# Performance work log

Measured on AMD Instinct MI355X. Metric: run time of the kernel, lower is better.

Reference implementation:

```python
import jax, jax.numpy as jnp
import numpy as np

D_MODEL = 1024
N_HEAD = 16
D_HEAD = D_MODEL // N_HEAD
NEG = -1e9


def setup_inputs() -> dict:
    key = jax.random.key(0)
    ks = jax.random.split(key, 11)
    B, T, C = 4, 2048, D_MODEL
    s = 1.0 / np.sqrt(C)
    return {
        "q": jax.random.normal(ks[0], (B, T, C), jnp.float32),
        "k": jax.random.normal(ks[1], (B, T, C), jnp.float32),
        "v": jax.random.normal(ks[2], (B, T, C), jnp.float32),
        "w_q": jax.random.normal(ks[3], (C, C), jnp.float32) * s,
        "b_q": jnp.zeros((C,), jnp.float32),
        "w_k": jax.random.normal(ks[4], (C, C), jnp.float32) * s,
        "b_k": jnp.zeros((C,), jnp.float32),
        "w_v": jax.random.normal(ks[5], (C, C), jnp.float32) * s,
        "b_v": jnp.zeros((C,), jnp.float32),
        "w_o": jax.random.normal(ks[6], (C, C), jnp.float32) * s,
        "b_o": jnp.zeros((C,), jnp.float32),
    }


def reference(q, k, v, w_q, b_q, w_k, b_k, w_v, b_v, w_o, b_o):
    B, T, C = q.shape
    # projections; weights stored as [in, out]
    qh = (q @ w_q + b_q).reshape(B, T, N_HEAD, D_HEAD).transpose(0, 2, 1, 3)
    kh = (k @ w_k + b_k).reshape(B, T, N_HEAD, D_HEAD).transpose(0, 2, 1, 3)
    vh = (v @ w_v + b_v).reshape(B, T, N_HEAD, D_HEAD).transpose(0, 2, 1, 3)
    scores = jnp.einsum("bhqd,bhkd->bhqk", qh, kh) / jnp.sqrt(
        jnp.asarray(D_HEAD, qh.dtype))
    causal = jnp.tril(jnp.ones((T, T), dtype=bool))  # [T,T]
    scores = jnp.where(causal[None, None], scores, NEG)
    attn = jax.nn.softmax(scores, axis=-1)
    out = jnp.einsum("bhqk,bhkd->bhqd", attn, vh)
    out = out.transpose(0, 2, 1, 3).reshape(B, T, C)
    return out @ w_o + b_o
```

## Files before the change

kernel.cpp:

```cpp
#include <hip/hip_runtime.h>
#include <hip/hip_bf16.h>
#include <cstdint>
#include <cstddef>

#define DEVI static __device__ __forceinline__

typedef __attribute__((ext_vector_type(8))) short short8;
typedef __attribute__((ext_vector_type(4))) float f32x4;

typedef __attribute__((address_space(1))) const unsigned int as1c_uint;
typedef __attribute__((address_space(3))) unsigned int as3_uint;

constexpr int Bn = 4, Tn = 2048, Cn = 1024, Hn = 16, Dn = 64;
constexpr int Mtot = Bn * Tn;
#define QSCALE (0.125f * 1.44269504088896340736f)

DEVI unsigned short f2bf(float f) {
  unsigned u = __float_as_uint(f);
  u += 0x7fffu + ((u >> 16) & 1u);
  return (unsigned short)(u >> 16);
}
DEVI unsigned short f2bf_t(float f) {
  return (unsigned short)(__float_as_uint(f) >> 16);
}

DEVI void async16(const void* g, void* l) {
  __builtin_amdgcn_global_load_lds((as1c_uint*)g, (as3_uint*)l, 16, 0, 0);
}

__global__ __launch_bounds__(256) void cvt3_kernel(
    const float4* __restrict__ i0, const float4* __restrict__ i1,
    const float4* __restrict__ i2, ushort4* __restrict__ o0,
    ushort4* __restrict__ o1, ushort4* __restrict__ o2, int n4, int zoff) {
  const int z = blockIdx.y + zoff;
  const float4* in = z == 0 ? i0 : z == 1 ? i1 : i2;
  ushort4* out = z == 0 ? o0 : z == 1 ? o1 : o2;
  const int stride = gridDim.x * blockDim.x;
  for (int i = blockIdx.x * blockDim.x + threadIdx.x; i < n4; i += stride) {
    float4 v = in[i];
    ushort4 o;
    o.x = f2bf(v.x); o.y = f2bf(v.y); o.z = f2bf(v.z); o.w = f2bf(v.w);
    out[i] = o;
  }
}

__global__ __launch_bounds__(256) void transpose_cvt4(
    const float* __restrict__ w0, const float* __restrict__ w1,
    const float* __restrict__ w2, const float* __restrict__ w3,
    unsigned short* __restrict__ o0, unsigned short* __restrict__ o1,
    unsigned short* __restrict__ o2, unsigned short* __restrict__ o3) {
  __shared__ float tile[32][33];
  const int z = blockIdx.z;
  const float* w = z == 0 ? w0 : z == 1 ? w1 : z == 2 ? w2 : w3;
  unsigned short* wT = z == 0 ? o0 : z == 1 ? o1 : z == 2 ? o2 : o3;
  int n0 = blockIdx.x * 32, k0 = blockIdx.y * 32;
  int tx = threadIdx.x, ty = threadIdx.y;
#pragma unroll
  for (int r = 0; r < 32; r += 8)
    tile[ty + r][tx] = w[(size_t)(k0 + ty + r) * Cn + n0 + tx];
  __syncthreads();
#pragma unroll
  for (int r = 0; r < 32; r += 8)
    wT[(size_t)(n0 + ty + r) * Cn + k0 + tx] = f2bf(tile[tx][ty + r]);
}

DEVI void gemm_core(const unsigned short* A, const unsigned short* BT, int K,
                    int m0, int n0, int tid, f32x4 acc[4][4]) {
  __shared__ unsigned short Alds[128 * 32];
  __shared__ unsigned short Blds[128 * 32];
  const int lane = tid & 63, w = tid >> 6;
  const int wm = w >> 1, wn = w & 1;
  const int l15 = lane & 15, l4 = lane >> 4;

  for (int k0 = 0; k0 < K; k0 += 32) {
    __syncthreads();
#pragma unroll
    for (int t = 0; t < 2; ++t) {
      int chunk = w * 2 + t;
      int row = chunk * 16 + (lane >> 2);
      int seg = lane & 3;
      async16(A + (size_t)(m0 + row) * K + k0 + seg * 8, &Alds[chunk * 512]);
      async16(BT + (size_t)(n0 + row) * K + k0 + seg * 8, &Blds[chunk * 512]);
    }
    __syncthreads();

    short8 af[4], bf[4];
#pragma unroll
    for (int i = 0; i < 4; ++i) {
      af[i] = *(const short8*)&Alds[(wm * 64 + i * 16 + l15) * 32 + l4 * 8];
      bf[i] = *(const short8*)&Blds[(wn * 64 + i * 16 + l15) * 32 + l4 * 8];
    }
#pragma unroll
    for (int i = 0; i < 4; ++i)
#pragma unroll
      for (int j = 0; j < 4; ++j)
        acc[i][j] = __builtin_amdgcn_mfma_f32_16x16x32_bf16(af[i], bf[j], acc[i][j], 0, 0, 0);
  }
}

__global__ __launch_bounds__(256) void gemm_qkv(
    const unsigned short* __restrict__ Aq, const unsigned short* __restrict__ Ak,
    const unsigned short* __restrict__ Av, const unsigned short* __restrict__ Bq,
    const unsigned short* __restrict__ Bk, const unsigned short* __restrict__ Bv,
    const float* __restrict__ bq, const float* __restrict__ bk,
    const float* __restrict__ bv, unsigned short* __restrict__ oq,
    unsigned short* __restrict__ ok, unsigned short* __restrict__ ov, int zoff) {
  const int z = blockIdx.z + zoff;
  const unsigned short* A = z == 0 ? Aq : z == 1 ? Ak : Av;
  const unsigned short* BT = z == 0 ? Bq : z == 1 ? Bk : Bv;
  const float* bias = z == 0 ? bq : z == 1 ? bk : bv;
  unsigned short* o = z == 0 ? oq : z == 1 ? ok : ov;

  const int tid = threadIdx.x;
  const int lane = tid & 63, w = tid >> 6;
  const int wm = w >> 1, wn = w & 1;
  const int l15 = lane & 15, l4 = lane >> 4;
  const int m0 = blockIdx.x * 128, n0 = blockIdx.y * 128;

  const f32x4 zf = {0.f, 0.f, 0.f, 0.f};
  f32x4 acc[4][4];
#pragma unroll
  for (int i = 0; i < 4; ++i)
#pragma unroll
    for (int j = 0; j < 4; ++j) acc[i][j] = zf;

  gemm_core(A, BT, Cn, m0, n0, tid, acc);

#pragma unroll
  for (int j = 0; j < 4; ++j) {
    int n = n0 + wn * 64 + j * 16 + l15;
    float bvl = bias[n];
    int h = n >> 6, d = n & 63;
#pragma unroll
    for (int i = 0; i < 4; ++i) {
      int mbase = m0 + wm * 64 + i * 16 + l4 * 4;
      if (z < 2) {
        float scale = z == 0 ? QSCALE : 1.f;
#pragma unroll
        for (int r = 0; r < 4; ++r) {
          int m = mbase + r;
          int b = m >> 11, t = m & 2047;
          o[((size_t)((b * Hn + h) * Tn + t)) * Dn + d] = f2bf((acc[i][j][r] + bvl) * scale);
        }
      } else {
        int b = mbase >> 11, t0 = mbase & 2047;
        ushort4 pk;
        pk.x = f2bf(acc[i][j][0] + bvl);
        pk.y = f2bf(acc[i][j][1] + bvl);
        pk.z = f2bf(acc[i][j][2] + bvl);
        pk.w = f2bf(acc[i][j][3] + bvl);
        *(ushort4*)&o[((size_t)((b * Hn + h) * Dn + d)) * Tn + t0] = pk;
      }
    }
  }
}

__global__ __launch_bounds__(256) void gemm_out(const unsigned short* __restrict__ A,
                                                const unsigned short* __restrict__ BT,
                                                const float* __restrict__ bias,
                                                float* __restrict__ o) {
  const int tid = threadIdx.x;
  const int lane = tid & 63, w = tid >> 6;
  const int wm = w >> 1, wn = w & 1;
  const int l15 = lane & 15, l4 = lane >> 4;
  const int m0 = blockIdx.x * 128, n0 = blockIdx.y * 128;

  const f32x4 zf = {0.f, 0.f, 0.f, 0.f};
  f32x4 acc[4][4];
#pragma unroll
  for (int i = 0; i < 4; ++i)
#pragma unroll
    for (int j = 0; j < 4; ++j) acc[i][j] = zf;

  gemm_core(A, BT, Cn, m0, n0, tid, acc);

#pragma unroll
  for (int j = 0; j < 4; ++j) {
    int n = n0 + wn * 64 + j * 16 + l15;
    float bvl = bias[n];
#pragma unroll
    for (int i = 0; i < 4; ++i) {
      int mbase = m0 + wm * 64 + i * 16 + l4 * 4;
#pragma unroll
      for (int r = 0; r < 4; ++r)
        o[(size_t)(mbase + r) * Cn + n] = acc[i][j][r] + bvl;
    }
  }
}

__global__ __launch_bounds__(512) void attn_kernel(const unsigned short* __restrict__ qh,
                                                   const unsigned short* __restrict__ kh,
                                                   const unsigned short* __restrict__ vt,
                                                   unsigned short* __restrict__ obf) {
  __shared__ unsigned short Ks[2][64 * 64];
  __shared__ unsigned short Vs[2][64 * 64];
  __shared__ unsigned short Ps[8][16 * 72];

  const int tid = threadIdx.x, lane = tid & 63, w = tid >> 6;
  const int l15 = lane & 15, l4 = lane >> 4;
  const int swz = l15 & 7;

  const int bid = blockIdx.x;
  const int j = bid >> 3;
  const int bh = (bid & 7) * 8 + (j & 7);
  const int pair = j >> 3;
  const unsigned short* qb = qh + (size_t)bh * Tn * Dn;
  const unsigned short* kb = kh + (size_t)bh * Tn * Dn;
  const unsigned short* vb = vt + (size_t)bh * Dn * Tn;
  const int b = bh >> 4, h = bh & 15;

  const int srow = lane >> 3, sslot = (lane & 7) ^ (lane >> 3);

  const f32x4 z = {0.f, 0.f, 0.f, 0.f};
  const short ob = (short)0x3F80;
  const short8 ones = {ob, ob, ob, ob, ob, ob, ob, ob};

#pragma unroll 1
  for (int half = 0; half < 2; ++half) {
    const int qt = half == 0 ? pair : 15 - pair;
    const int q0 = qt * 128;
    const int qrow = q0 + w * 16 + l15;

    short8 qf0 = *(const short8*)(qb + (size_t)qrow * Dn + l4 * 8);
    short8 qf1 = *(const short8*)(qb + (size_t)qrow * Dn + 32 + l4 * 8);

    f32x4 o[4];
#pragma unroll
    for (int nd = 0; nd < 4; ++nd) o[nd] = z;
    f32x4 osum = z;

    const int nt = (q0 >> 6) + 2;
    const int ntw = ((q0 + w * 16 + 15) >> 6) + 1;

    {
      const unsigned short* ksrc = kb + (size_t)(w * 8 + srow) * Dn + sslot * 8;
      const unsigned short* vsrc = vb + (size_t)(w * 8 + srow) * Tn + sslot * 8;
      async16(ksrc, &Ks[0][w * 512]);
      async16(vsrc, &Vs[0][w * 512]);
    }

#pragma unroll 1
    for (int t = 0; t < nt; ++t) {
      const int cur = t & 1;
      if (t + 1 < nt) {
        const int kv1 = (t + 1) * 64;
        const unsigned short* ksrc = kb + (size_t)(kv1 + w * 8 + srow) * Dn + sslot * 8;
        const unsigned short* vsrc = vb + (size_t)(w * 8 + srow) * Tn + kv1 + sslot * 8;
        async16(ksrc, &Ks[cur ^ 1][w * 512]);
        async16(vsrc, &Vs[cur ^ 1][w * 512]);
        asm volatile("s_waitcnt vmcnt(2)" ::: "memory");
      } else {
        asm volatile("s_waitcnt vmcnt(0)" ::: "memory");
      }
      __builtin_amdgcn_s_barrier();
      __builtin_amdgcn_sched_barrier(0);

      if (t < ntw) {
        const unsigned short* Kc = &Ks[cur][0];
        const unsigned short* Vc = &Vs[cur][0];

        f32x4 s[4];
#pragma unroll
        for (int ni = 0; ni < 4; ++ni) s[ni] = z;
        __builtin_amdgcn_s_setprio(1);
#pragma unroll
        for (int ni = 0; ni < 4; ++ni) {
          const int rb = (ni * 16 + l15) * 64;
          short8 kf0 = *(const short8*)&Kc[rb + ((l4 ^ swz) * 8)];
          short8 kf1 = *(const short8*)&Kc[rb + (((4 + l4) ^ swz) * 8)];
          s[ni] = __builtin_amdgcn_mfma_f32_16x16x32_bf16(kf0, qf0, s[ni], 0, 0, 0);
          s[ni] = __builtin_amdgcn_mfma_f32_16x16x32_bf16(kf1, qf1, s[ni], 0, 0, 0);
        }
        __builtin_amdgcn_s_setprio(0);

        short8 vf[8];
#pragma unroll
        for (int nd = 0; nd < 4; ++nd) {
          const int rb = (nd * 16 + l15) * 64;
          vf[nd * 2]     = *(const short8*)&Vc[rb + ((l4 ^ swz) * 8)];
          vf[nd * 2 + 1] = *(const short8*)&Vc[rb + (((4 + l4) ^ swz) * 8)];
        }

        const int kq = qrow - t * 64;
        const bool edge = (t * 64 + 63 > q0 + w * 16);
        if (!edge) {
#pragma unroll
          for (int ni = 0; ni < 4; ++ni) {
            ushort4 pk;
#pragma unroll
            for (int r = 0; r < 4; ++r)
              ((unsigned short*)&pk)[r] = f2bf_t(__builtin_amdgcn_exp2f(s[ni][r]));
            *(ushort4*)&Ps[w][l15 * 72 + ni * 16 + l4 * 4] = pk;
          }
        } else {
#pragma unroll
          for (int ni = 0; ni < 4; ++ni) {
            ushort4 pk;
#pragma unroll
            for (int r = 0; r < 4; ++r) {
              float e = __builtin_amdgcn_exp2f(s[ni][r]);
              if ((ni * 16 + l4 * 4 + r) > kq) e = 0.f;
              ((unsigned short*)&pk)[r] = f2bf_t(e);
            }
            *(ushort4*)&Ps[w][l15 * 72 + ni * 16 + l4 * 4] = pk;
          }
        }
        asm volatile("s_waitcnt lgkmcnt(0)" ::: "memory");
        __builtin_amdgcn_sched_barrier(0);

        short8 pf0 = *(const short8*)&Ps[w][l15 * 72 + l4 * 8];
        short8 pf1 = *(const short8*)&Ps[w][l15 * 72 + 32 + l4 * 8];
        __builtin_amdgcn_s_setprio(1);
        osum = __builtin_amdgcn_mfma_f32_16x16x32_bf16(pf0, ones, osum, 0, 0, 0);
        osum = __builtin_amdgcn_mfma_f32_16x16x32_bf16(pf1, ones, osum, 0, 0, 0);
#pragma unroll
        for (int nd = 0; nd < 4; ++nd) {
          o[nd] = __builtin_amdgcn_mfma_f32_16x16x32_bf16(pf0, vf[nd * 2], o[nd], 0, 0, 0);
          o[nd] = __builtin_amdgcn_mfma_f32_16x16x32_bf16(pf1, vf[nd * 2 + 1], o[nd], 0, 0, 0);
        }
        __builtin_amdgcn_s_setprio(0);
      }

      __builtin_amdgcn_sched_barrier(0);
      __builtin_amdgcn_s_barrier();
    }

#pragma unroll
    for (int r = 0; r < 4; ++r) {
      float inv = __builtin_amdgcn_rcpf(osum[r]);
      int tq = q0 + w * 16 + l4 * 4 + r;
      size_t base = ((size_t)(b * Tn + tq)) * Cn + h * 64;
#pragma unroll
      for (int nd = 0; nd < 4; ++nd)
        obf[base + nd * 16 + l15] = f2bf(o[nd][r] * inv);
    }
  }
}

extern "C" void kernel_launch(void* const* d_in, const int* in_sizes, int n_in,
                              void* d_out, int out_size, void* d_ws, size_t ws_size,
                              hipStream_t stream) {
  const float* q   = (const float*)d_in[0];
  const float* k   = (const float*)d_in[1];
  const float* v   = (const float*)d_in[2];
  const float* w_q = (const float*)d_in[3];
  const float* b_q = (const float*)d_in[4];
  const float* w_k = (const float*)d_in[5];
  const float* b_k = (const float*)d_in[6];
  const float* w_v = (const float*)d_in[7];
  const float* b_v = (const float*)d_in[8];
  const float* w_o = (const float*)d_in[9];
  const float* b_o = (const float*)d_in[10];

  char* ws = (char*)d_ws;
  const size_t MB = 1u << 20;
  const bool big = ws_size >= 104 * MB;
  const int n4 = Mtot * Cn / 4;
  dim3 gg(Mtot / 128, Cn / 128, 1);

  unsigned short *xq, *xk, *xv, *qhp, *khp, *vtp, *wqT, *wkT, *wvT, *woT;
  if (big) {
    xq  = (unsigned short*)(ws);
    xk  = (unsigned short*)(ws + 16 * MB);
    xv  = (unsigned short*)(ws + 32 * MB);
    qhp = (unsigned short*)(ws + 48 * MB);
    khp = (unsigned short*)(ws + 64 * MB);
    vtp = (unsigned short*)(ws + 80 * MB);
    wqT = (unsigned short*)(ws + 96 * MB);
    wkT = (unsigned short*)(ws + 98 * MB);
    wvT = (unsigned short*)(ws + 100 * MB);
    woT = (unsigned short*)(ws + 102 * MB);
  } else {
    xq = xk = xv = (unsigned short*)(ws);
    wqT = (unsigned short*)(ws + 16 * MB);
    wkT = (unsigned short*)(ws + 18 * MB);
    wvT = (unsigned short*)(ws + 20 * MB);
    woT = (unsigned short*)(ws + 22 * MB);
    qhp = (unsigned short*)(ws + 24 * MB);
    khp = (unsigned short*)(ws + 40 * MB);
    vtp = (unsigned short*)(ws + 56 * MB);
  }
  unsigned short* aout = xq;

  transpose_cvt4<<<dim3(32, 32, 4), dim3(32, 8), 0, stream>>>(
      w_q, w_k, w_v, w_o, wqT, wkT, wvT, woT);

  if (big) {
    cvt3_kernel<<<dim3(2048, 3), 256, 0, stream>>>(
        (const float4*)q, (const float4*)k, (const float4*)v,
        (ushort4*)xq, (ushort4*)xk, (ushort4*)xv, n4, 0);
    dim3 g3(Mtot / 128, Cn / 128, 3);
    gemm_qkv<<<g3, 256, 0, stream>>>(xq, xk, xv, wqT, wkT, wvT,
                                     b_q, b_k, b_v, qhp, khp, vtp, 0);
  } else {
    for (int z = 0; z < 3; ++z) {
      cvt3_kernel<<<dim3(2048, 1), 256, 0, stream>>>(
          (const float4*)q, (const float4*)k, (const float4*)v,
          (ushort4*)xq, (ushort4*)xq, (ushort4*)xq, n4, z);
      gemm_qkv<<<gg, 256, 0, stream>>>(xq, xq, xq, wqT, wkT, wvT,
                                       b_q, b_k, b_v, qhp, khp, vtp, z);
    }
  }

  attn_kernel<<<512, 512, 0, stream>>>(qhp, khp, vtp, aout);

  gemm_out<<<gg, 256, 0, stream>>>(aout, woT, b_o, (float*)d_out);
}
```

Before: 182.4 us.

## Replace GEMM core with 256x256 double-buffered swizzled-LDS tile kernel

Replaces the 128x128 single-buffered GEMM core with a 256x256 tile per 512-thread block. It uses a 64-wide K step, double-buffered async LDS staging with XOR-swizzled columns, prefetch two stages ahead, and s_setprio around the MFMA bursts. Block IDs are remapped so neighbouring blocks share tiles. The aim is more data reuse per byte loaded, fewer bank conflicts, and load latency hidden behind compute. The cost is heavy register and LDS use (128 KB per block) and fewer blocks: 128 per GEMM, or 384 for the fused QKV launch.

```diff
diff --git a/kernel.cpp b/kernel.cpp
--- a/kernel.cpp
+++ b/kernel.cpp
@@ -64,41 +64,92 @@
     wT[(size_t)(n0 + ty + r) * Cn + k0 + tx] = f2bf(tile[tx][ty + r]);
 }
 
-DEVI void gemm_core(const unsigned short* A, const unsigned short* BT, int K,
-                    int m0, int n0, int tid, f32x4 acc[4][4]) {
-  __shared__ unsigned short Alds[128 * 32];
-  __shared__ unsigned short Blds[128 * 32];
+DEVI void stage256(const unsigned short* __restrict__ g, int ld, int m0, int k0,
+                   unsigned short* lds, int w, int lane) {
+#pragma unroll
+  for (int j = 0; j < 4; ++j) {
+    int s = j * 512 + w * 64 + lane;
+    int row = s >> 3;
+    int col = ((s & 7) ^ (row & 7)) * 8;
+    async16(g + (size_t)(m0 + row) * ld + k0 + col,
+            lds + (size_t)(j * 512 + w * 64) * 8);
+  }
+}
+
+DEVI void gemm8p_core(const unsigned short* __restrict__ A,
+                      const unsigned short* __restrict__ BT, int K,
+                      int m0, int n0, int tid, f32x4 (&acc)[8][4]) {
+  __shared__ unsigned short As[2][256 * 64];
+  __shared__ unsigned short Bs[2][256 * 64];
   const int lane = tid & 63, w = tid >> 6;
-  const int wm = w >> 1, wn = w & 1;
+  const int wm = w >> 2, wn = w & 3;
   const int l15 = lane & 15, l4 = lane >> 4;
-
-  for (int k0 = 0; k0 < K; k0 += 32) {
-    __syncthreads();
-#pragma unroll
-    for (int t = 0; t < 2; ++t) {
-      int chunk = w * 2 + t;
-      int row = chunk * 16 + (lane >> 2);
-      int seg = lane & 3;
-      async16(A + (size_t)(m0 + row) * K + k0 + seg * 8, &Alds[chunk * 512]);
-      async16(BT + (size_t)(n0 + row) * K + k0 + seg * 8, &Blds[chunk * 512]);
-    }
-    __syncthreads();
-
-    short8 af[4], bf[4];
-#pragma unroll
-    for (int i = 0; i < 4; ++i) {
-      af[i] = *(const short8*)&Alds[(wm * 64 + i * 16 + l15) * 32 + l4 * 8];
-      bf[i] = *(const short8*)&Blds[(wn * 64 + i * 16 + l15) * 32 + l4 * 8];
-    }
-#pragma unroll
-    for (int i = 0; i < 4; ++i)
-#pragma unroll
-      for (int j = 0; j < 4; ++j)
-        acc[i][j] = __builtin_amdgcn_mfma_f32_16x16x32_bf16(af[i], bf[j], acc[i][j], 0, 0, 0);
-  }
-}
-
-__global__ __launch_bounds__(256) void gemm_qkv(
+  const int NT = K >> 6;
+
+  stage256(A, K, m0, 0, As[0], w, lane);
+  stage256(BT, K, n0, 0, Bs[0], w, lane);
+  stage256(A, K, m0, 64, As[1], w, lane);
+  stage256(BT, K, n0, 64, Bs[1], w, lane);
+
+  const int arow = wm * 128 + l15;
+  const int brow = wn * 64 + l15;
+
+#pragma unroll 1
+  for (int kt = 0; kt < NT; ++kt) {
+    const int c = kt & 1;
+    if (kt + 1 < NT) {
+      asm volatile("s_waitcnt vmcnt(8)" ::: "memory");
+    } else {
+      asm volatile("s_waitcnt vmcnt(0)" ::: "memory");
+    }
+    __builtin_amdgcn_s_barrier();
+    __builtin_amdgcn_sched_barrier(0);
+    const unsigned short* Ab = As[c];
+    const unsigned short* Bb = Bs[c];
+
+    short8 bfr[4][2];
+#pragma unroll
+    for (int j = 0; j < 4; ++j)
+#pragma unroll
+      for (int kk = 0; kk < 2; ++kk) {
+        int r = brow + j * 16;
+        bfr[j][kk] = *(const short8*)&Bb[r * 64 + (((kk * 4 + l4) ^ (r & 7)) * 8)];
+      }
+
+#pragma unroll
+    for (int ph = 0; ph < 4; ++ph) {
+      short8 af[2][2];
+#pragma unroll
+      for (int ii = 0; ii < 2; ++ii)
+#pragma unroll
+        for (int kk = 0; kk < 2; ++kk) {
+          int r = arow + (ph * 2 + ii) * 16;
+          af[ii][kk] = *(const short8*)&Ab[r * 64 + (((kk * 4 + l4) ^ (r & 7)) * 8)];
+        }
+      if (ph == 3) {
+        asm volatile("s_waitcnt lgkmcnt(0)" ::: "memory");
+        __builtin_amdgcn_s_barrier();
+        __builtin_amdgcn_sched_barrier(0);
+        if (kt + 2 < NT) {
+          stage256(A, K, m0, (kt + 2) * 64, As[c], w, lane);
+          stage256(BT, K, n0, (kt + 2) * 64, Bs[c], w, lane);
+        }
+      }
+      __builtin_amdgcn_s_setprio(1);
+#pragma unroll
+      for (int ii = 0; ii < 2; ++ii)
+#pragma unroll
+        for (int j = 0; j < 4; ++j)
+#pragma unroll
+          for (int kk = 0; kk < 2; ++kk)
+            acc[ph * 2 + ii][j] = __builtin_amdgcn_mfma_f32_16x16x32_bf16(
+                af[ii][kk], bfr[j][kk], acc[ph * 2 + ii][j], 0, 0, 0);
+      __builtin_amdgcn_s_setprio(0);
+    }
+  }
+}
+
+__global__ __launch_bounds__(512, 2) void gemm8p_qkv(
     const unsigned short* __restrict__ Aq, const unsigned short* __restrict__ Ak,
     const unsigned short* __restrict__ Av, const unsigned short* __restrict__ Bq,
     const unsigned short* __restrict__ Bk, const unsigned short* __restrict__ Bv,
@@ -113,18 +164,20 @@
 
   const int tid = threadIdx.x;
   const int lane = tid & 63, w = tid >> 6;
-  const int wm = w >> 1, wn = w & 1;
+  const int wm = w >> 2, wn = w & 3;
   const int l15 = lane & 15, l4 = lane >> 4;
-  const int m0 = blockIdx.x * 128, n0 = blockIdx.y * 128;
+  const int fid = blockIdx.y * 32 + blockIdx.x;
+  const int swz = (fid & 7) * 16 + (fid >> 3);
+  const int m0 = (swz & 31) * 256, n0 = (swz >> 5) * 256;
 
   const f32x4 zf = {0.f, 0.f, 0.f, 0.f};
-  f32x4 acc[4][4];
-#pragma unroll
-  for (int i = 0; i < 4; ++i)
+  f32x4 acc[8][4];
+#pragma unroll
+  for (int i = 0; i < 8; ++i)
 #pragma unroll
     for (int j = 0; j < 4; ++j) acc[i][j] = zf;
 
-  gemm_core(A, BT, Cn, m0, n0, tid, acc);
+  gemm8p_core(A, BT, Cn, m0, n0, tid, acc);
 
 #pragma unroll
   for (int j = 0; j < 4; ++j) {
@@ -132,8 +185,8 @@
     float bvl = bias[n];
     int h = n >> 6, d = n & 63;
 #pragma unroll
-    for (int i = 0; i < 4; ++i) {
-      int mbase = m0 + wm * 64 + i * 16 + l4 * 4;
+    for (int i = 0; i < 8; ++i) {
+      int mbase = m0 + wm * 128 + i * 16 + l4 * 4;
       if (z < 2) {
         float scale = z == 0 ? QSCALE : 1.f;
 #pragma unroll
@@ -155,32 +208,33 @@
   }
 }
 
-__global__ __launch_bounds__(256) void gemm_out(const unsigned short* __restrict__ A,
-                                                const unsigned short* __restrict__ BT,
-                                                const float* __restrict__ bias,
-                                                float* __restrict__ o) {
+__global__ __launch_bounds__(512, 2) void gemm8p_out(
+    const unsigned short* __restrict__ A, const unsigned short* __restrict__ BT,
+    const float* __restrict__ bias, float* __restrict__ o) {
   const int tid = threadIdx.x;
   const int lane = tid & 63, w = tid >> 6;
-  const int wm = w >> 1, wn = w & 1;
+  const int wm = w >> 2, wn = w & 3;
   const int l15 = lane & 15, l4 = lane >> 4;
-  const int m0 = blockIdx.x * 128, n0 = blockIdx.y * 128;
+  const int fid = blockIdx.y * 32 + blockIdx.x;
+  const int swz = (fid & 7) * 16 + (fid >> 3);
+  const int m0 = (swz & 31) * 256, n0 = (swz >> 5) * 256;
 
   const f32x4 zf = {0.f, 0.f, 0.f, 0.f};
-  f32x4 acc[4][4];
-#pragma unroll
-  for (int i = 0; i < 4; ++i)
+  f32x4 acc[8][4];
+#pragma unroll
+  for (int i = 0; i < 8; ++i)
 #pragma unroll
     for (int j = 0; j < 4; ++j) acc[i][j] = zf;
 
-  gemm_core(A, BT, Cn, m0, n0, tid, acc);
+  gemm8p_core(A, BT, Cn, m0, n0, tid, acc);
 
 #pragma unroll
   for (int j = 0; j < 4; ++j) {
     int n = n0 + wn * 64 + j * 16 + l15;
     float bvl = bias[n];
 #pragma unroll
-    for (int i = 0; i < 4; ++i) {
-      int mbase = m0 + wm * 64 + i * 16 + l4 * 4;
+    for (int i = 0; i < 8; ++i) {
+      int mbase = m0 + wm * 128 + i * 16 + l4 * 4;
 #pragma unroll
       for (int r = 0; r < 4; ++r)
         o[(size_t)(mbase + r) * Cn + n] = acc[i][j][r] + bvl;
@@ -356,7 +410,7 @@
   const size_t MB = 1u << 20;
   const bool big = ws_size >= 104 * MB;
   const int n4 = Mtot * Cn / 4;
-  dim3 gg(Mtot / 128, Cn / 128, 1);
+  dim3 gg(Mtot / 256, Cn / 256, 1);
 
   unsigned short *xq, *xk, *xv, *qhp, *khp, *vtp, *wqT, *wkT, *wvT, *woT;
   if (big) {
@@ -389,20 +443,20 @@
     cvt3_kernel<<<dim3(2048, 3), 256, 0, stream>>>(
         (const float4*)q, (const float4*)k, (const float4*)v,
         (ushort4*)xq, (ushort4*)xk, (ushort4*)xv, n4, 0);
-    dim3 g3(Mtot / 128, Cn / 128, 3);
-    gemm_qkv<<<g3, 256, 0, stream>>>(xq, xk, xv, wqT, wkT, wvT,
-                                     b_q, b_k, b_v, qhp, khp, vtp, 0);
+    dim3 g3(Mtot / 256, Cn / 256, 3);
+    gemm8p_qkv<<<g3, 512, 0, stream>>>(xq, xk, xv, wqT, wkT, wvT,
+                                       b_q, b_k, b_v, qhp, khp, vtp, 0);
   } else {
     for (int z = 0; z < 3; ++z) {
       cvt3_kernel<<<dim3(2048, 1), 256, 0, stream>>>(
           (const float4*)q, (const float4*)k, (const float4*)v,
           (ushort4*)xq, (ushort4*)xq, (ushort4*)xq, n4, z);
-      gemm_qkv<<<gg, 256, 0, stream>>>(xq, xq, xq, wqT, wkT, wvT,
-                                       b_q, b_k, b_v, qhp, khp, vtp, z);
+      gemm8p_qkv<<<gg, 512, 0, stream>>>(xq, xq, xq, wqT, wkT, wvT,
+                                         b_q, b_k, b_v, qhp, khp, vtp, z);
     }
   }
 
   attn_kernel<<<512, 512, 0, stream>>>(qhp, khp, vtp, aout);
 
-  gemm_out<<<gg, 256, 0, stream>>>(aout, woT, b_o, (float*)d_out);
-}
+  gemm8p_out<<<gg, 512, 0, stream>>>(aout, woT, b_o, (float*)d_out);
+}
```

After: 195.6 us. 1.07x slower.

## Replace tiled GEMMs with strip-resident projection kernels using pre-fragmented weights

Applied to the files above, without the earlier changes.

The 128x128 LDS-tiled GEMMs for the QKV and output projections are replaced by kernels that stage a full 64x1024 activation strip in swizzled LDS once. Each wave then streams weight fragments straight from global memory into registers with double buffering. The weight transpose kernel now writes weights in an MFMA-fragment-ordered layout so those loads are coalesced, and the epilogues use vectorized stores. This removes the per-K-step syncthreads and the repeated A/B tile staging, at the cost of 128KB of LDS per block (lower occupancy) and more global traffic for the weights, which relies on L2 caching them.

```diff
diff --git a/kernel.cpp b/kernel.cpp
--- a/kernel.cpp
+++ b/kernel.cpp
@@ -59,111 +59,156 @@
   for (int r = 0; r < 32; r += 8)
     tile[ty + r][tx] = w[(size_t)(k0 + ty + r) * Cn + n0 + tx];
   __syncthreads();
-#pragma unroll
-  for (int r = 0; r < 32; r += 8)
-    wT[(size_t)(n0 + ty + r) * Cn + k0 + tx] = f2bf(tile[tx][ty + r]);
-}
-
-DEVI void gemm_core(const unsigned short* A, const unsigned short* BT, int K,
-                    int m0, int n0, int tid, f32x4 acc[4][4]) {
-  __shared__ unsigned short Alds[128 * 32];
-  __shared__ unsigned short Blds[128 * 32];
-  const int lane = tid & 63, w = tid >> 6;
-  const int wm = w >> 1, wn = w & 1;
+  const int t = ty * 32 + tx;
+  const int n_l = t >> 3;
+  const int kq = (t & 7) * 4;
+  const int n = n0 + n_l, k = k0 + kq;
+  ushort4 pk;
+#pragma unroll
+  for (int e = 0; e < 4; ++e) ((unsigned short*)&pk)[e] = f2bf(tile[kq + e][n_l]);
+  size_t idx = (size_t)((((n >> 4) * 32 + (k >> 5)) * 64 + ((k >> 3) & 3) * 16 + (n & 15))) * 8 + (k & 7);
+  *(ushort4*)&wT[idx] = pk;
+}
+
+DEVI short8 xfrag(const unsigned short* Xlds, int i, int kc, int l15, int l4) {
+  int row = i * 16 + l15;
+  return *(const short8*)&Xlds[row * 1024 + (((kc * 4 + l4) ^ (row & 7)) * 8)];
+}
+
+template <int NJ, bool SWAP>
+DEVI void proj_core(const unsigned short* __restrict__ wF,
+                    const unsigned short* Xlds, int njb, int lane,
+                    f32x4 (&acc)[4][NJ]) {
   const int l15 = lane & 15, l4 = lane >> 4;
-
-  for (int k0 = 0; k0 < K; k0 += 32) {
-    __syncthreads();
-#pragma unroll
-    for (int t = 0; t < 2; ++t) {
-      int chunk = w * 2 + t;
-      int row = chunk * 16 + (lane >> 2);
-      int seg = lane & 3;
-      async16(A + (size_t)(m0 + row) * K + k0 + seg * 8, &Alds[chunk * 512]);
-      async16(BT + (size_t)(n0 + row) * K + k0 + seg * 8, &Blds[chunk * 512]);
-    }
-    __syncthreads();
-
-    short8 af[4], bf[4];
-#pragma unroll
-    for (int i = 0; i < 4; ++i) {
-      af[i] = *(const short8*)&Alds[(wm * 64 + i * 16 + l15) * 32 + l4 * 8];
-      bf[i] = *(const short8*)&Blds[(wn * 64 + i * 16 + l15) * 32 + l4 * 8];
-    }
+  const short8* wp = (const short8*)wF;
+  short8 wfA[NJ], wfB[NJ];
+#pragma unroll
+  for (int j = 0; j < NJ; ++j) wfA[j] = wp[((njb + j) * 32) * 64 + lane];
+#pragma unroll 1
+  for (int kc = 0; kc < 32; kc += 2) {
+#pragma unroll
+    for (int j = 0; j < NJ; ++j) wfB[j] = wp[((njb + j) * 32 + kc + 1) * 64 + lane];
+    short8 xf[4];
+#pragma unroll
+    for (int i = 0; i < 4; ++i) xf[i] = xfrag(Xlds, i, kc, l15, l4);
 #pragma unroll
     for (int i = 0; i < 4; ++i)
 #pragma unroll
-      for (int j = 0; j < 4; ++j)
-        acc[i][j] = __builtin_amdgcn_mfma_f32_16x16x32_bf16(af[i], bf[j], acc[i][j], 0, 0, 0);
-  }
-}
-
-__global__ __launch_bounds__(256) void gemm_qkv(
-    const unsigned short* __restrict__ Aq, const unsigned short* __restrict__ Ak,
-    const unsigned short* __restrict__ Av, const unsigned short* __restrict__ Bq,
-    const unsigned short* __restrict__ Bk, const unsigned short* __restrict__ Bv,
+      for (int j = 0; j < NJ; ++j)
+        acc[i][j] = SWAP
+            ? __builtin_amdgcn_mfma_f32_16x16x32_bf16(xf[i], wfA[j], acc[i][j], 0, 0, 0)
+            : __builtin_amdgcn_mfma_f32_16x16x32_bf16(wfA[j], xf[i], acc[i][j], 0, 0, 0);
+    if (kc + 2 < 32) {
+#pragma unroll
+      for (int j = 0; j < NJ; ++j) wfA[j] = wp[((njb + j) * 32 + kc + 2) * 64 + lane];
+    }
+#pragma unroll
+    for (int i = 0; i < 4; ++i) xf[i] = xfrag(Xlds, i, kc + 1, l15, l4);
+#pragma unroll
+    for (int i = 0; i < 4; ++i)
+#pragma unroll
+      for (int j = 0; j < NJ; ++j)
+        acc[i][j] = SWAP
+            ? __builtin_amdgcn_mfma_f32_16x16x32_bf16(xf[i], wfB[j], acc[i][j], 0, 0, 0)
+            : __builtin_amdgcn_mfma_f32_16x16x32_bf16(wfB[j], xf[i], acc[i][j], 0, 0, 0);
+  }
+}
+
+DEVI void stage_strip(const unsigned short* __restrict__ src, int m0,
+                      unsigned short* Xlds, int tid) {
+#pragma unroll
+  for (int it = 0; it < 16; ++it) {
+    int s = it * 512 + tid;
+    int row = s >> 7, sl = s & 127;
+    async16(src + (size_t)(m0 + row) * Cn + ((sl ^ (row & 7)) * 8),
+            Xlds + (size_t)(it * 512 + (tid & ~63)) * 8);
+  }
+}
+
+__global__ __launch_bounds__(512, 2) void proj_qkv(
+    const unsigned short* __restrict__ xq, const unsigned short* __restrict__ xk,
+    const unsigned short* __restrict__ xv, const unsigned short* __restrict__ wFq,
+    const unsigned short* __restrict__ wFk, const unsigned short* __restrict__ wFv,
     const float* __restrict__ bq, const float* __restrict__ bk,
     const float* __restrict__ bv, unsigned short* __restrict__ oq,
     unsigned short* __restrict__ ok, unsigned short* __restrict__ ov, int zoff) {
-  const int z = blockIdx.z + zoff;
-  const unsigned short* A = z == 0 ? Aq : z == 1 ? Ak : Av;
-  const unsigned short* BT = z == 0 ? Bq : z == 1 ? Bk : Bv;
+  __shared__ unsigned short Xlds[64 * 1024];
+  const int tid = threadIdx.x, lane = tid & 63, w = tid >> 6;
+  const int l15 = lane & 15, l4 = lane >> 4;
+  const int bid = blockIdx.x;
+  const int z = zoff + (bid >> 7);
+  const int m0 = (bid & 127) * 64;
+  const unsigned short* xz = z == 0 ? xq : z == 1 ? xk : xv;
+  const unsigned short* wF = z == 0 ? wFq : z == 1 ? wFk : wFv;
   const float* bias = z == 0 ? bq : z == 1 ? bk : bv;
-  unsigned short* o = z == 0 ? oq : z == 1 ? ok : ov;
-
-  const int tid = threadIdx.x;
-  const int lane = tid & 63, w = tid >> 6;
-  const int wm = w >> 1, wn = w & 1;
-  const int l15 = lane & 15, l4 = lane >> 4;
-  const int m0 = blockIdx.x * 128, n0 = blockIdx.y * 128;
+
+  stage_strip(xz, m0, Xlds, tid);
+  __syncthreads();
 
   const f32x4 zf = {0.f, 0.f, 0.f, 0.f};
-  f32x4 acc[4][4];
+  f32x4 acc[4][8];
 #pragma unroll
   for (int i = 0; i < 4; ++i)
 #pragma unroll
-    for (int j = 0; j < 4; ++j) acc[i][j] = zf;
-
-  gemm_core(A, BT, Cn, m0, n0, tid, acc);
-
-#pragma unroll
-  for (int j = 0; j < 4; ++j) {
-    int n = n0 + wn * 64 + j * 16 + l15;
-    float bvl = bias[n];
-    int h = n >> 6, d = n & 63;
-#pragma unroll
-    for (int i = 0; i < 4; ++i) {
-      int mbase = m0 + wm * 64 + i * 16 + l4 * 4;
-      if (z < 2) {
-        float scale = z == 0 ? QSCALE : 1.f;
-#pragma unroll
-        for (int r = 0; r < 4; ++r) {
-          int m = mbase + r;
-          int b = m >> 11, t = m & 2047;
-          o[((size_t)((b * Hn + h) * Tn + t)) * Dn + d] = f2bf((acc[i][j][r] + bvl) * scale);
-        }
-      } else {
-        int b = mbase >> 11, t0 = mbase & 2047;
+    for (int j = 0; j < 8; ++j) acc[i][j] = zf;
+
+  const int njb = w * 8;
+  if (z < 2)
+    proj_core<8, false>(wF, Xlds, njb, lane, acc);
+  else
+    proj_core<8, true>(wF, Xlds, njb, lane, acc);
+
+  const int b = m0 >> 11, t0loc = m0 & 2047;
+  if (z < 2) {
+    unsigned short* o = z == 0 ? oq : ok;
+    const float scale = z == 0 ? QSCALE : 1.f;
+#pragma unroll
+    for (int j = 0; j < 8; ++j) {
+      int ng = njb + j;
+      int h = ng >> 2, d0 = (ng & 3) * 16 + l4 * 4;
+      float4 bv4 = *(const float4*)&bias[ng * 16 + l4 * 4];
+#pragma unroll
+      for (int i = 0; i < 4; ++i) {
+        int t = t0loc + i * 16 + l15;
+        ushort4 pk;
+        pk.x = f2bf((acc[i][j][0] + bv4.x) * scale);
+        pk.y = f2bf((acc[i][j][1] + bv4.y) * scale);
+        pk.z = f2bf((acc[i][j][2] + bv4.z) * scale);
+        pk.w = f2bf((acc[i][j][3] + bv4.w) * scale);
+        *(ushort4*)&o[((size_t)((b * Hn + h) * Tn + t)) * Dn + d0] = pk;
+      }
+    }
+  } else {
+#pragma unroll
+    for (int j = 0; j < 8; ++j) {
+      int n = (njb + j) * 16 + l15;
+      int h = n >> 6, d = n & 63;
+      float bvl = bias[n];
+#pragma unroll
+      for (int i = 0; i < 4; ++i) {
+        int t0 = t0loc + i * 16 + l4 * 4;
         ushort4 pk;
         pk.x = f2bf(acc[i][j][0] + bvl);
         pk.y = f2bf(acc[i][j][1] + bvl);
         pk.z = f2bf(acc[i][j][2] + bvl);
         pk.w = f2bf(acc[i][j][3] + bvl);
-        *(ushort4*)&o[((size_t)((b * Hn + h) * Dn + d)) * Tn + t0] = pk;
+        *(ushort4*)&ov[((size_t)((b * Hn + h) * Dn + d)) * Tn + t0] = pk;
       }
     }
   }
 }
 
-__global__ __launch_bounds__(256) void gemm_out(const unsigned short* __restrict__ A,
-                                                const unsigned short* __restrict__ BT,
-                                                const float* __restrict__ bias,
-                                                float* __restrict__ o) {
-  const int tid = threadIdx.x;
-  const int lane = tid & 63, w = tid >> 6;
-  const int wm = w >> 1, wn = w & 1;
+__global__ __launch_bounds__(512, 2) void proj_out(
+    const unsigned short* __restrict__ A, const unsigned short* __restrict__ wFo,
+    const float* __restrict__ bias, float* __restrict__ o) {
+  __shared__ unsigned short Xlds[64 * 1024];
+  const int tid = threadIdx.x, lane = tid & 63, w = tid >> 6;
   const int l15 = lane & 15, l4 = lane >> 4;
-  const int m0 = blockIdx.x * 128, n0 = blockIdx.y * 128;
+  const int bid = blockIdx.x;
+  const int m0 = (bid >> 1) * 64, nh = bid & 1;
+
+  stage_strip(A, m0, Xlds, tid);
+  __syncthreads();
 
   const f32x4 zf = {0.f, 0.f, 0.f, 0.f};
   f32x4 acc[4][4];
@@ -172,18 +217,22 @@
 #pragma unroll
     for (int j = 0; j < 4; ++j) acc[i][j] = zf;
 
-  gemm_core(A, BT, Cn, m0, n0, tid, acc);
+  const int njb = nh * 32 + w * 4;
+  proj_core<4, false>(wFo, Xlds, njb, lane, acc);
 
 #pragma unroll
   for (int j = 0; j < 4; ++j) {
-    int n = n0 + wn * 64 + j * 16 + l15;
-    float bvl = bias[n];
+    int ng = njb + j;
+    float4 bv4 = *(const float4*)&bias[ng * 16 + l4 * 4];
 #pragma unroll
     for (int i = 0; i < 4; ++i) {
-      int mbase = m0 + wm * 64 + i * 16 + l4 * 4;
-#pragma unroll
-      for (int r = 0; r < 4; ++r)
-        o[(size_t)(mbase + r) * Cn + n] = acc[i][j][r] + bvl;
+      int m = m0 + i * 16 + l15;
+      float4 ov4;
+      ov4.x = acc[i][j][0] + bv4.x;
+      ov4.y = acc[i][j][1] + bv4.y;
+      ov4.z = acc[i][j][2] + bv4.z;
+      ov4.w = acc[i][j][3] + bv4.w;
+      *(float4*)&o[(size_t)m * Cn + ng * 16 + l4 * 4] = ov4;
     }
   }
 }
@@ -356,7 +405,6 @@
   const size_t MB = 1u << 20;
   const bool big = ws_size >= 104 * MB;
   const int n4 = Mtot * Cn / 4;
-  dim3 gg(Mtot / 128, Cn / 128, 1);
 
   unsigned short *xq, *xk, *xv, *qhp, *khp, *vtp, *wqT, *wkT, *wvT, *woT;
   if (big) {
@@ -389,20 +437,19 @@
     cvt3_kernel<<<dim3(2048, 3), 256, 0, stream>>>(
         (const float4*)q, (const float4*)k, (const float4*)v,
         (ushort4*)xq, (ushort4*)xk, (ushort4*)xv, n4, 0);
-    dim3 g3(Mtot / 128, Cn / 128, 3);
-    gemm_qkv<<<g3, 256, 0, stream>>>(xq, xk, xv, wqT, wkT, wvT,
-                                     b_q, b_k, b_v, qhp, khp, vtp, 0);
+    proj_qkv<<<384, 512, 0, stream>>>(xq, xk, xv, wqT, wkT, wvT,
+                                      b_q, b_k, b_v, qhp, khp, vtp, 0);
   } else {
     for (int z = 0; z < 3; ++z) {
       cvt3_kernel<<<dim3(2048, 1), 256, 0, stream>>>(
           (const float4*)q, (const float4*)k, (const float4*)v,
           (ushort4*)xq, (ushort4*)xq, (ushort4*)xq, n4, z);
-      gemm_qkv<<<gg, 256, 0, stream>>>(xq, xq, xq, wqT, wkT, wvT,
-                                       b_q, b_k, b_v, qhp, khp, vtp, z);
+      proj_qkv<<<128, 512, 0, stream>>>(xq, xq, xq, wqT, wkT, wvT,
+                                        b_q, b_k, b_v, qhp, khp, vtp, z);
     }
   }
 
   attn_kernel<<<512, 512, 0, stream>>>(qhp, khp, vtp, aout);
 
-  gemm_out<<<gg, 256, 0, stream>>>(aout, woT, b_o, (float*)d_out);
-}
+  proj_out<<<256, 512, 0, stream>>>(aout, woT, b_o, (float*)d_out);
+}
```

New measurement: 181.2 us. Within noise of the previous version (-0.7%).
